# Optimization experiments

Measured on AMD Instinct MI355X. Metric: run time of the kernel, lower is better.

## Reference

```python
import jax, jax.numpy as jnp
import numpy as np

M = 50000   # eval points
N = 1024    # gaussians
EPS = 1e-6


def setup_inputs() -> dict:
    key = jax.random.key(0)
    k1, k2, k3 = jax.random.split(key, 3)
    points = jax.random.uniform(k1, (M, 3), dtype=jnp.float32)          # normalized coords in [0,1)
    positions = jax.random.uniform(k2, (N, 3), dtype=jnp.float32)       # torch.rand init
    log_scales = jnp.full((N, 3), -3.0, dtype=jnp.float32)              # torch.full(..., -3.0)
    intensities = jax.random.uniform(k3, (N,), dtype=jnp.float32) * 0.5  # torch.rand * 0.5
    return {"points": points, "positions": positions,
            "log_scales": log_scales, "intensities": intensities}


def reference(points, positions, log_scales, intensities):
    # Faithful translation of FastGaussianModel._eval_gaussians
    scales = jnp.exp(log_scales)                      # [N,3]
    inv_var = 1.0 / (scales ** 2 + EPS)               # [N,3]
    diff = points[:, None, :] - positions[None, :, :] # [M,N,3]
    quad = jnp.einsum('mnd,nd->mn', diff * diff, inv_var)  # [M,N]
    gauss = jnp.exp(-0.5 * quad)                      # [M,N]
    values = gauss @ intensities                      # [M]
    return values
```

## Files before the change

kernel.cpp:

```cpp
#include <hip/hip_runtime.h>


typedef float v2f __attribute__((ext_vector_type(2)));

constexpr int BLOCK         = 128;
constexpr int WAVES_PER_BLK = 2;
constexpr int PTS_PER_LANE  = 4;
constexpr int TILE_PTS      = 64 * PTS_PER_LANE;
constexpr int SLICE_GROUPS  = 32;
constexpr int TOTAL_SLICES  = SLICE_GROUPS * WAVES_PER_BLK;
constexpr int RECF          = 16;
constexpr int MAXPPS        = 48;
constexpr float KLN  = -0.7213475204444817f;
constexpr float FEPS = 1e-6f;


template <int PAIRS>
__device__ __forceinline__ void sweep_fast(const v2f* __restrict__ cp, int pairs,
                                           const float* px, const float* py,
                                           const float* pz, const float* pp,
                                           v2f* acc) {
    const int n = PAIRS > 0 ? PAIRS : pairs;
    #pragma unroll
    for (int i = 0; i < n; ++i) {
        v2f A0 = cp[0], A1 = cp[1], A2 = cp[2], C = cp[3], W = cp[4];
        cp += 8;
        #pragma unroll
        for (int j = 0; j < PTS_PER_LANE; ++j) {
            v2f t = C + (v2f){pp[j], pp[j]};
            t = __builtin_elementwise_fma(A2, (v2f){pz[j], pz[j]}, t);
            t = __builtin_elementwise_fma(A1, (v2f){py[j], py[j]}, t);
            t = __builtin_elementwise_fma(A0, (v2f){px[j], px[j]}, t);
            v2f g;
            g.x = __builtin_amdgcn_exp2f(t.x);
            g.y = __builtin_amdgcn_exp2f(t.y);
            acc[j] = __builtin_elementwise_fma(g, W, acc[j]);
        }
    }
}

template <int PAIRS>
__device__ __forceinline__ void sweep_full(const v2f* __restrict__ cp, int pairs,
                                           const float* px, const float* py,
                                           const float* pz, v2f* acc) {
    const int n = PAIRS > 0 ? PAIRS : pairs;
    #pragma unroll 2
    for (int i = 0; i < n; ++i) {
        v2f A0 = cp[0], A1 = cp[1], A2 = cp[2], C = cp[3], W = cp[4];
        v2f B0 = cp[5], B1 = cp[6], B2 = cp[7];
        cp += 8;
        #pragma unroll
        for (int j = 0; j < PTS_PER_LANE; ++j) {
            v2f t = __builtin_elementwise_fma(B0, (v2f){px[j]*px[j], px[j]*px[j]}, C);
            t = __builtin_elementwise_fma(B1, (v2f){py[j]*py[j], py[j]*py[j]}, t);
            t = __builtin_elementwise_fma(B2, (v2f){pz[j]*pz[j], pz[j]*pz[j]}, t);
            t = __builtin_elementwise_fma(A2, (v2f){pz[j], pz[j]}, t);
            t = __builtin_elementwise_fma(A1, (v2f){py[j], py[j]}, t);
            t = __builtin_elementwise_fma(A0, (v2f){px[j], px[j]}, t);
            v2f g;
            g.x = __builtin_amdgcn_exp2f(t.x);
            g.y = __builtin_amdgcn_exp2f(t.y);
            acc[j] = __builtin_elementwise_fma(g, W, acc[j]);
        }
    }
}

template <int PAIRS>
__global__ __launch_bounds__(BLOCK) void fgm_main(
        const float* __restrict__ points,
        const float* __restrict__ positions,
        const float* __restrict__ log_scales,
        const float* __restrict__ intensities,
        float* __restrict__ out,
        int M, int N, int pairsPerSlice) {
    constexpr int CPAIRS = PAIRS > 0 ? PAIRS : MAXPPS;
    __shared__ __align__(16) float recs[WAVES_PER_BLK][CPAIRS * RECF];
    __shared__ float red[WAVES_PER_BLK][TILE_PTS];

    const int lane = threadIdx.x & 63;
    const int wave = __builtin_amdgcn_readfirstlane(threadIdx.x >> 6);
    const int tileBase = blockIdx.x * TILE_PTS;
    const int slice = blockIdx.y * WAVES_PER_BLK + wave;
    const int PPS = PAIRS > 0 ? PAIRS : pairsPerSlice;

    const float r0 = KLN / (__expf(2.0f * log_scales[0]) + FEPS);
    const float r1 = KLN / (__expf(2.0f * log_scales[1]) + FEPS);
    const float r2 = KLN / (__expf(2.0f * log_scales[2]) + FEPS);

    float px[PTS_PER_LANE], py[PTS_PER_LANE], pz[PTS_PER_LANE], pp[PTS_PER_LANE];
    v2f acc[PTS_PER_LANE];
    #pragma unroll
    for (int j = 0; j < PTS_PER_LANE; ++j) {
        int m = tileBase + lane + 64 * j;
        float x = 0.f, y = 0.f, z = 0.f;
        if (m < M) { x = points[3*m+0]; y = points[3*m+1]; z = points[3*m+2]; }
        px[j] = x;  py[j] = y;  pz[j] = z;
        pp[j] = r0*x*x + r1*y*y + r2*z*z;
        acc[j] = (v2f){0.f, 0.f};
    }

    for (int base = 0; base < PPS; base += CPAIRS) {
        const int cnt = (PPS - base < CPAIRS) ? (PPS - base) : CPAIRS;

        bool ok = true;
        for (int p = lane; p < cnt; p += 64) {
            float va[2][8];
            #pragma unroll
            for (int h = 0; h < 2; ++h) {
                int n = (slice * PPS + base + p) * 2 + h;
                float a0=0.f,a1=0.f,a2=0.f,b0=0.f,b1=0.f,b2=0.f,c=0.f,w=0.f;
                if (n < N) {
                    float q0 = positions[3*n+0], q1 = positions[3*n+1], q2 = positions[3*n+2];
                    b0 = KLN / (__expf(2.0f*log_scales[3*n+0]) + FEPS);
                    b1 = KLN / (__expf(2.0f*log_scales[3*n+1]) + FEPS);
                    b2 = KLN / (__expf(2.0f*log_scales[3*n+2]) + FEPS);
                    a0 = -2.f*b0*q0;  a1 = -2.f*b1*q1;  a2 = -2.f*b2*q2;
                    c  = b0*q0*q0 + b1*q1*q1 + b2*q2*q2;
                    w  = intensities[n];
                    if (b0 != r0 || b1 != r1 || b2 != r2) ok = false;
                }
                va[h][0]=a0; va[h][1]=a1; va[h][2]=a2; va[h][3]=b0;
                va[h][4]=b1; va[h][5]=b2; va[h][6]=c;  va[h][7]=w;
            }
            v2f* r = (v2f*)&recs[wave][p * RECF];
            r[0] = (v2f){va[0][0], va[1][0]};
            r[1] = (v2f){va[0][1], va[1][1]};
            r[2] = (v2f){va[0][2], va[1][2]};
            r[3] = (v2f){va[0][6], va[1][6]};
            r[4] = (v2f){va[0][7], va[1][7]};
            r[5] = (v2f){va[0][3], va[1][3]};
            r[6] = (v2f){va[0][4], va[1][4]};
            r[7] = (v2f){va[0][5], va[1][5]};
        }
        const bool fast = __all(ok);
        __syncthreads();

        const v2f* cp = (const v2f*)recs[wave];
        if (fast) sweep_fast<PAIRS>(cp, cnt, px, py, pz, pp, acc);
        else      sweep_full<PAIRS>(cp, cnt, px, py, pz, acc);
    }

    #pragma unroll
    for (int j = 0; j < PTS_PER_LANE; ++j)
        red[wave][lane + 64*j] = acc[j].x + acc[j].y;
    __syncthreads();

    for (int p = threadIdx.x; p < TILE_PTS; p += BLOCK) {
        int m = tileBase + p;
        if (m < M) atomicAdd(&out[m], red[0][p] + red[1][p]);
    }
}

extern "C" void kernel_launch(void* const* d_in, const int* in_sizes, int n_in,
                              void* d_out, int out_size, void* d_ws, size_t ws_size,
                              hipStream_t stream) {
    const float* points      = (const float*)d_in[0];
    const float* positions   = (const float*)d_in[1];
    const float* log_scales  = (const float*)d_in[2];
    const float* intensities = (const float*)d_in[3];
    int M = in_sizes[0] / 3;
    int N = in_sizes[3];

    int Npairs = (N + 1) / 2;
    int PPS    = (Npairs + TOTAL_SLICES - 1) / TOTAL_SLICES;

    hipMemsetAsync(d_out, 0, (size_t)out_size * sizeof(float), stream);

    int tiles = (M + TILE_PTS - 1) / TILE_PTS;
    dim3 grid(tiles, SLICE_GROUPS);
    if (PPS == 8) {
        fgm_main<8><<<grid, BLOCK, 0, stream>>>(points, positions, log_scales,
                                                intensities, (float*)d_out, M, N, PPS);
    } else {
        fgm_main<0><<<grid, BLOCK, 0, stream>>>(points, positions, log_scales,
                                                intensities, (float*)d_out, M, N, PPS);
    }
}
```

Measured before the change: 75.14 us.

## Replace atomic accumulation with per-slice partial buffers and a separate reduce kernel

The sweep kernel now writes per-slice partial sums with float4 stores into a workspace buffer, and a second kernel sums the 32 slices. This removes the memset, the shared-memory block reduction and the global atomics. Each lane now owns 4 contiguous points loaded with float4 reads, and Gaussian parameters are read in pairs with vector loads. Slice groups are halved, which doubles the pairs per slice and halves the grid. In exchange there is an extra kernel launch and roughly 6.4 MB of partial-sum traffic through the workspace.

```diff
diff --git a/kernel.cpp b/kernel.cpp
--- a/kernel.cpp
+++ b/kernel.cpp
@@ -5,9 +5,8 @@
 
 constexpr int BLOCK         = 128;
 constexpr int WAVES_PER_BLK = 2;
-constexpr int PTS_PER_LANE  = 4;
-constexpr int TILE_PTS      = 64 * PTS_PER_LANE;
-constexpr int SLICE_GROUPS  = 32;
+constexpr int TILE_PTS      = 256;
+constexpr int SLICE_GROUPS  = 16;
 constexpr int TOTAL_SLICES  = SLICE_GROUPS * WAVES_PER_BLK;
 constexpr int RECF          = 16;
 constexpr int MAXPPS        = 48;
@@ -26,7 +25,7 @@
         v2f A0 = cp[0], A1 = cp[1], A2 = cp[2], C = cp[3], W = cp[4];
         cp += 8;
         #pragma unroll
-        for (int j = 0; j < PTS_PER_LANE; ++j) {
+        for (int j = 0; j < 4; ++j) {
             v2f t = C + (v2f){pp[j], pp[j]};
             t = __builtin_elementwise_fma(A2, (v2f){pz[j], pz[j]}, t);
             t = __builtin_elementwise_fma(A1, (v2f){py[j], py[j]}, t);
@@ -50,7 +49,7 @@
         v2f B0 = cp[5], B1 = cp[6], B2 = cp[7];
         cp += 8;
         #pragma unroll
-        for (int j = 0; j < PTS_PER_LANE; ++j) {
+        for (int j = 0; j < 4; ++j) {
             v2f t = __builtin_elementwise_fma(B0, (v2f){px[j]*px[j], px[j]*px[j]}, C);
             t = __builtin_elementwise_fma(B1, (v2f){py[j]*py[j], py[j]*py[j]}, t);
             t = __builtin_elementwise_fma(B2, (v2f){pz[j]*pz[j], pz[j]*pz[j]}, t);
@@ -66,71 +65,93 @@
 }
 
 template <int PAIRS>
-__global__ __launch_bounds__(BLOCK) void fgm_main(
+__global__ __launch_bounds__(BLOCK) void fgm_sweep(
         const float* __restrict__ points,
         const float* __restrict__ positions,
         const float* __restrict__ log_scales,
         const float* __restrict__ intensities,
-        float* __restrict__ out,
-        int M, int N, int pairsPerSlice) {
+        float* __restrict__ part,
+        int M, int Mpad, int N, int pairsPerSlice) {
     constexpr int CPAIRS = PAIRS > 0 ? PAIRS : MAXPPS;
     __shared__ __align__(16) float recs[WAVES_PER_BLK][CPAIRS * RECF];
-    __shared__ float red[WAVES_PER_BLK][TILE_PTS];
-
-    const int lane = threadIdx.x & 63;
-    const int wave = __builtin_amdgcn_readfirstlane(threadIdx.x >> 6);
-    const int tileBase = blockIdx.x * TILE_PTS;
+
+    const int lane  = threadIdx.x & 63;
+    const int wave  = __builtin_amdgcn_readfirstlane(threadIdx.x >> 6);
     const int slice = blockIdx.y * WAVES_PER_BLK + wave;
-    const int PPS = PAIRS > 0 ? PAIRS : pairsPerSlice;
+    const int PPS   = PAIRS > 0 ? PAIRS : pairsPerSlice;
+    const int m0    = blockIdx.x * TILE_PTS + 4 * lane;
 
     const float r0 = KLN / (__expf(2.0f * log_scales[0]) + FEPS);
     const float r1 = KLN / (__expf(2.0f * log_scales[1]) + FEPS);
     const float r2 = KLN / (__expf(2.0f * log_scales[2]) + FEPS);
 
-    float px[PTS_PER_LANE], py[PTS_PER_LANE], pz[PTS_PER_LANE], pp[PTS_PER_LANE];
-    v2f acc[PTS_PER_LANE];
+    float px[4], py[4], pz[4], pp[4];
+    if (m0 + 4 <= M) {
+        const float4* p4 = (const float4*)(points + 3 * (size_t)m0);
+        float4 f0 = p4[0], f1 = p4[1], f2 = p4[2];
+        px[0] = f0.x; py[0] = f0.y; pz[0] = f0.z;
+        px[1] = f0.w; py[1] = f1.x; pz[1] = f1.y;
+        px[2] = f1.z; py[2] = f1.w; pz[2] = f2.x;
+        px[3] = f2.y; py[3] = f2.z; pz[3] = f2.w;
+    } else {
+        #pragma unroll
+        for (int j = 0; j < 4; ++j) {
+            int m = m0 + j;
+            float x = 0.f, y = 0.f, z = 0.f;
+            if (m < M) { x = points[3*m+0]; y = points[3*m+1]; z = points[3*m+2]; }
+            px[j] = x; py[j] = y; pz[j] = z;
+        }
+    }
+    v2f acc[4];
     #pragma unroll
-    for (int j = 0; j < PTS_PER_LANE; ++j) {
-        int m = tileBase + lane + 64 * j;
-        float x = 0.f, y = 0.f, z = 0.f;
-        if (m < M) { x = points[3*m+0]; y = points[3*m+1]; z = points[3*m+2]; }
-        px[j] = x;  py[j] = y;  pz[j] = z;
-        pp[j] = r0*x*x + r1*y*y + r2*z*z;
+    for (int j = 0; j < 4; ++j) {
+        pp[j] = r0*px[j]*px[j] + r1*py[j]*py[j] + r2*pz[j]*pz[j];
         acc[j] = (v2f){0.f, 0.f};
     }
 
+    const int sliceBase = slice * PPS;
     for (int base = 0; base < PPS; base += CPAIRS) {
         const int cnt = (PPS - base < CPAIRS) ? (PPS - base) : CPAIRS;
 
         bool ok = true;
         for (int p = lane; p < cnt; p += 64) {
+            const int g = (sliceBase + base + p) * 2;
+            float q[6] = {0,0,0,0,0,0}, l[6] = {0,0,0,0,0,0}, w[2] = {0,0};
+            bool val[2] = {g < N, g + 1 < N};
+            if (val[1]) {
+                const v2f* q2 = (const v2f*)(positions  + 3 * (size_t)g);
+                const v2f* l2 = (const v2f*)(log_scales + 3 * (size_t)g);
+                v2f Q01 = q2[0], Q23 = q2[1], Q45 = q2[2];
+                v2f L01 = l2[0], L23 = l2[1], L45 = l2[2];
+                v2f W01 = *(const v2f*)(intensities + g);
+                q[0]=Q01.x; q[1]=Q01.y; q[2]=Q23.x; q[3]=Q23.y; q[4]=Q45.x; q[5]=Q45.y;
+                l[0]=L01.x; l[1]=L01.y; l[2]=L23.x; l[3]=L23.y; l[4]=L45.x; l[5]=L45.y;
+                w[0]=W01.x; w[1]=W01.y;
+            } else if (val[0]) {
+                q[0]=positions[3*g+0]; q[1]=positions[3*g+1]; q[2]=positions[3*g+2];
+                l[0]=log_scales[3*g+0]; l[1]=log_scales[3*g+1]; l[2]=log_scales[3*g+2];
+                w[0]=intensities[g];
+            }
             float va[2][8];
             #pragma unroll
             for (int h = 0; h < 2; ++h) {
-                int n = (slice * PPS + base + p) * 2 + h;
-                float a0=0.f,a1=0.f,a2=0.f,b0=0.f,b1=0.f,b2=0.f,c=0.f,w=0.f;
-                if (n < N) {
-                    float q0 = positions[3*n+0], q1 = positions[3*n+1], q2 = positions[3*n+2];
-                    b0 = KLN / (__expf(2.0f*log_scales[3*n+0]) + FEPS);
-                    b1 = KLN / (__expf(2.0f*log_scales[3*n+1]) + FEPS);
-                    b2 = KLN / (__expf(2.0f*log_scales[3*n+2]) + FEPS);
-                    a0 = -2.f*b0*q0;  a1 = -2.f*b1*q1;  a2 = -2.f*b2*q2;
-                    c  = b0*q0*q0 + b1*q1*q1 + b2*q2*q2;
-                    w  = intensities[n];
+                float a0=0.f,a1=0.f,a2=0.f,b0=0.f,b1=0.f,b2=0.f,c=0.f,wt=0.f;
+                if (val[h]) {
+                    b0 = KLN / (__expf(2.0f*l[3*h+0]) + FEPS);
+                    b1 = KLN / (__expf(2.0f*l[3*h+1]) + FEPS);
+                    b2 = KLN / (__expf(2.0f*l[3*h+2]) + FEPS);
+                    a0 = -2.f*b0*q[3*h+0];  a1 = -2.f*b1*q[3*h+1];  a2 = -2.f*b2*q[3*h+2];
+                    c  = b0*q[3*h+0]*q[3*h+0] + b1*q[3*h+1]*q[3*h+1]
+                       + b2*q[3*h+2]*q[3*h+2];
+                    wt = w[h];
                     if (b0 != r0 || b1 != r1 || b2 != r2) ok = false;
                 }
-                va[h][0]=a0; va[h][1]=a1; va[h][2]=a2; va[h][3]=b0;
-                va[h][4]=b1; va[h][5]=b2; va[h][6]=c;  va[h][7]=w;
+                va[h][0]=a0; va[h][1]=a1; va[h][2]=a2; va[h][3]=c;
+                va[h][4]=wt; va[h][5]=b0; va[h][6]=b1; va[h][7]=b2;
             }
             v2f* r = (v2f*)&recs[wave][p * RECF];
-            r[0] = (v2f){va[0][0], va[1][0]};
-            r[1] = (v2f){va[0][1], va[1][1]};
-            r[2] = (v2f){va[0][2], va[1][2]};
-            r[3] = (v2f){va[0][6], va[1][6]};
-            r[4] = (v2f){va[0][7], va[1][7]};
-            r[5] = (v2f){va[0][3], va[1][3]};
-            r[6] = (v2f){va[0][4], va[1][4]};
-            r[7] = (v2f){va[0][5], va[1][5]};
+            #pragma unroll
+            for (int k = 0; k < 8; ++k) r[k] = (v2f){va[0][k], va[1][k]};
         }
         const bool fast = __all(ok);
         __syncthreads();
@@ -140,15 +161,23 @@
         else      sweep_full<PAIRS>(cp, cnt, px, py, pz, acc);
     }
 
-    #pragma unroll
-    for (int j = 0; j < PTS_PER_LANE; ++j)
-        red[wave][lane + 64*j] = acc[j].x + acc[j].y;
-    __syncthreads();
-
-    for (int p = threadIdx.x; p < TILE_PTS; p += BLOCK) {
-        int m = tileBase + p;
-        if (m < M) atomicAdd(&out[m], red[0][p] + red[1][p]);
-    }
+    float4 vout = make_float4(acc[0].x + acc[0].y, acc[1].x + acc[1].y,
+                              acc[2].x + acc[2].y, acc[3].x + acc[3].y);
+    *(float4*)(part + (size_t)slice * Mpad + m0) = vout;
+}
+
+__global__ __launch_bounds__(256) void fgm_reduce(const float* __restrict__ part,
+                                                  float* __restrict__ out,
+                                                  int M, int Mpad, int out_n) {
+    int m = blockIdx.x * 256 + threadIdx.x;
+    if (m >= out_n) return;
+    float s = 0.f;
+    if (m < M) {
+        #pragma unroll
+        for (int sl = 0; sl < TOTAL_SLICES; ++sl)
+            s += part[(size_t)sl * Mpad + m];
+    }
+    out[m] = s;
 }
 
 extern "C" void kernel_launch(void* const* d_in, const int* in_sizes, int n_in,
@@ -163,16 +192,20 @@
 
     int Npairs = (N + 1) / 2;
     int PPS    = (Npairs + TOTAL_SLICES - 1) / TOTAL_SLICES;
-
-    hipMemsetAsync(d_out, 0, (size_t)out_size * sizeof(float), stream);
-
-    int tiles = (M + TILE_PTS - 1) / TILE_PTS;
+    int tiles  = (M + TILE_PTS - 1) / TILE_PTS;
+    int Mpad   = tiles * TILE_PTS;
+
+    float* part = (float*)d_ws;
+
     dim3 grid(tiles, SLICE_GROUPS);
-    if (PPS == 8) {
-        fgm_main<8><<<grid, BLOCK, 0, stream>>>(points, positions, log_scales,
-                                                intensities, (float*)d_out, M, N, PPS);
+    if (PPS == 16) {
+        fgm_sweep<16><<<grid, BLOCK, 0, stream>>>(points, positions, log_scales,
+                                                  intensities, part, M, Mpad, N, PPS);
     } else {
-        fgm_main<0><<<grid, BLOCK, 0, stream>>>(points, positions, log_scales,
-                                                intensities, (float*)d_out, M, N, PPS);
-    }
-}
+        fgm_sweep<0><<<grid, BLOCK, 0, stream>>>(points, positions, log_scales,
+                                                 intensities, part, M, Mpad, N, PPS);
+    }
+
+    int rblocks = (out_size + 255) / 256;
+    fgm_reduce<<<rblocks, 256, 0, stream>>>(part, (float*)d_out, M, Mpad, out_size);
+}
```

Result: no change. 73.76 us (-1.8%).
